# Performance work log

Hardware: AMD Instinct MI355X
Metric: run time of the kernel (lower is better)

## Reference

```python
import jax, jax.numpy as jnp
import numpy as np

STRIDE = 1
PAD = 1
DIL = 1


def setup_inputs() -> dict:
    key = jax.random.key(0)
    k1, k2, k3 = jax.random.split(key, 3)
    N, Cin, H, W = 8, 128, 96, 96
    Cout, Kh, Kw = 256, 3, 3
    inp = jax.random.normal(k1, (N, Cin, H, W), dtype=jnp.float32)
    # offset channels: 2*Kh*Kw per offset group (1 group), layout (dy, dx) pairs
    offset = jax.random.normal(k2, (N, 2 * Kh * Kw, H, W), dtype=jnp.float32)
    weight = jax.random.normal(k3, (Cout, Cin, Kh, Kw), dtype=jnp.float32) * 0.05
    return {"input": inp, "offset": offset, "weight": weight}


def _deform_conv(inp, offset, weight):
    N, Cin, H, W = inp.shape
    Cout, _, Kh, Kw = weight.shape
    K = Kh * Kw
    Ho = (H + 2 * PAD - DIL * (Kh - 1) - 1) // STRIDE + 1
    Wo = (W + 2 * PAD - DIL * (Kw - 1) - 1) // STRIDE + 1

    # base sampling grid (before learned offsets)
    hs = jnp.arange(Ho, dtype=inp.dtype) * STRIDE - PAD          # [Ho]
    ws = jnp.arange(Wo, dtype=inp.dtype) * STRIDE - PAD          # [Wo]
    ky, kx = jnp.meshgrid(jnp.arange(Kh, dtype=inp.dtype) * DIL,
                          jnp.arange(Kw, dtype=inp.dtype) * DIL,
                          indexing="ij")
    ky = ky.reshape(K)
    kx = kx.reshape(K)

    off = offset.reshape(N, K, 2, Ho, Wo)                        # pairs (dy, dx)
    py = hs[None, None, :, None] + ky[None, :, None, None] + off[:, :, 0]  # [N,K,Ho,Wo]
    px = ws[None, None, None, :] + kx[None, :, None, None] + off[:, :, 1]  # [N,K,Ho,Wo]

    y0 = jnp.floor(py)
    x0 = jnp.floor(px)
    ly = py - y0   # fractional parts
    lx = px - x0
    y0i = y0.astype(jnp.int32)
    x0i = x0.astype(jnp.int32)

    img = inp.transpose(0, 2, 3, 1)                              # [N,H,W,Cin]
    bidx = jnp.arange(N)[:, None, None, None]

    def gather(yi, xi):
        valid = (yi >= 0) & (yi < H) & (xi >= 0) & (xi < W)
        yc = jnp.clip(yi, 0, H - 1)
        xc = jnp.clip(xi, 0, W - 1)
        v = img[bidx, yc, xc]                                    # [N,K,Ho,Wo,Cin]
        return v * valid[..., None].astype(img.dtype)

    v00 = gather(y0i, x0i)
    v01 = gather(y0i, x0i + 1)
    v10 = gather(y0i + 1, x0i)
    v11 = gather(y0i + 1, x0i + 1)

    wy, wx = ly[..., None], lx[..., None]
    samp = (v00 * (1 - wy) * (1 - wx) + v01 * (1 - wy) * wx
            + v10 * wy * (1 - wx) + v11 * wy * wx)               # [N,K,Ho,Wo,Cin]

    w2 = weight.reshape(Cout, Cin, K)
    return jnp.einsum("nkhwc,ock->nohw", samp, w2)               # [N,Cout,Ho,Wo]


def reference(input, offset, weight):
    return _deform_conv(input, offset, weight)
```

## Files before the change

kernel.cpp:

```cpp
#include <hip/hip_runtime.h>
#include <hip/hip_bf16.h>

#define NN   8
#define CIN  128
#define HH   96
#define WW   96
#define COUT 256
#define KK   9
#define HO   96
#define WO   96
#define PTOT (NN*HO*WO)
#define BM   64
#define KTOT (CIN*KK)
#define KSTEPS (KTOT/32)

typedef short bf16x8 __attribute__((ext_vector_type(8)));
typedef float f32x4  __attribute__((ext_vector_type(4)));
typedef float f32x2  __attribute__((ext_vector_type(2)));

__device__ __forceinline__ float blo(unsigned u) { return __uint_as_float(u << 16); }
__device__ __forceinline__ float bhi(unsigned u) { return __uint_as_float(u & 0xffff0000u); }
__device__ __forceinline__ f32x2 unpk(unsigned u) {
    f32x2 r;
    r.x = __uint_as_float(u << 16);
    r.y = __uint_as_float(u & 0xffff0000u);
    return r;
}
__device__ __forceinline__ unsigned pack_bf2(float a, float b) {
    unsigned ua = __float_as_uint(a); ua += 0x7fffu + ((ua >> 16) & 1u);
    unsigned ub = __float_as_uint(b); ub += 0x7fffu + ((ub >> 16) & 1u);
    return (ua >> 16) | (ub & 0xffff0000u);
}
__device__ __forceinline__ unsigned short f2b(float a) {
    unsigned ua = __float_as_uint(a); ua += 0x7fffu + ((ua >> 16) & 1u);
    return (unsigned short)(ua >> 16);
}

__global__ __launch_bounds__(256) void to_nhwc_bf16(const float* __restrict__ in,
                                                    unsigned short* __restrict__ outp) {
    __shared__ float tile[CIN * 97];
    const int ny = blockIdx.x;
    const int n = ny / HH, y = ny - n * HH;
    const float* src = in + (size_t)n * CIN * HH * WW + (size_t)y * WW;
    for (int i = threadIdx.x; i < CIN * WW; i += 256) {
        int c = i / WW, x = i - c * WW;
        tile[c * 97 + x] = src[(size_t)c * HH * WW + x];
    }
    __syncthreads();
    unsigned* dst = (unsigned*)(outp + (size_t)ny * WW * CIN);
    for (int i = threadIdx.x; i < (WW * CIN) / 2; i += 256) {
        int c2 = (i & 63) * 2;
        int x  = i >> 6;
        dst[x * (CIN / 2) + (c2 >> 1)] = pack_bf2(tile[c2 * 97 + x], tile[(c2 + 1) * 97 + x]);
    }
}

__global__ __launch_bounds__(256) void w_pack(const float* __restrict__ w,
                                              unsigned short* __restrict__ wp) {
    int idx = blockIdx.x * 256 + threadIdx.x;
    if (idx >= KSTEPS * 16 * 64 * 8) return;
    int j  = idx & 7;
    int l  = (idx >> 3) & 63;
    int cb = (idx >> 9) & 15;
    int ks = idx >> 13;
    int co  = cb * 16 + (l & 15);
    int kg  = ks * 32 + ((l >> 4) * 8) + j;
    int tap = kg >> 7;
    int cin = kg & 127;
    wp[idx] = f2b(w[((size_t)co * CIN + cin) * KK + tap]);
}

#define GEOM_BYTES 6912
#define LDS_BYTES  39680
#define BUF0 6912
#define BUF1 23296

__global__ __launch_bounds__(256, 4) void deform_mfma(
    const unsigned short* __restrict__ imgB,
    const float*          __restrict__ off,
    const unsigned short* __restrict__ wPack,
    float*                __restrict__ out)
{
    __shared__ __align__(16) char smem[LDS_BYTES];
    unsigned* gOff = (unsigned*)smem;
    unsigned* gW0  = (unsigned*)(smem + 2304);
    unsigned* gW1  = (unsigned*)(smem + 4608);

    const int t    = threadIdx.x;
    const int lane = t & 63;
    const int wv   = t >> 6;

    const int bid  = ((blockIdx.x & 7) * ((PTOT / BM) >> 3)) + (blockIdx.x >> 3);

    const int p0   = bid * BM;
    const int nb   = p0 / (HO * WO);
    const int p0rem = p0 - nb * (HO * WO);

    for (int i = t; i < KK * BM; i += 256) {
        int tap = i >> 6, m = i & 63;
        int plin = p0rem + m;
        int ho = plin / WO, wo = plin - ho * WO;
        int kh = tap / 3, kw = tap - kh * 3;
        const float* ob = off + ((size_t)nb * 2 * KK + 2 * tap) * (HO * WO) + plin;
        float py = (float)(ho - 1 + kh) + ob[0];
        float px = (float)(wo - 1 + kw) + ob[HO * WO];
        float y0f = floorf(py), x0f = floorf(px);
        float ly = py - y0f, lx = px - x0f;
        int y0 = (int)y0f, x0 = (int)x0f;

        bool vy0 = (unsigned)y0 < (unsigned)HH;
        bool vy1 = (unsigned)(y0 + 1) < (unsigned)HH;
        bool vx0 = (unsigned)x0 < (unsigned)WW;
        bool vx1 = (unsigned)(x0 + 1) < (unsigned)WW;
        int yc0 = min(max(y0, 0), HH - 1);
        int yc1 = min(max(y0 + 1, 0), HH - 1);
        int xc0 = min(max(x0, 0), WW - 1);
        int xc1 = min(max(x0 + 1, 0), WW - 1);

        float w11 = ly * lx;
        float w10 = ly - w11;
        float w01 = lx - w11;
        float w00 = 1.f - ly - lx + w11;
        w00 = (vy0 && vx0) ? w00 : 0.f;
        w01 = (vy0 && vx1) ? w01 : 0.f;
        w10 = (vy1 && vx0) ? w10 : 0.f;
        w11 = (vy1 && vx1) ? w11 : 0.f;

        unsigned byte00 = (unsigned)(yc0 * WW + xc0) * (CIN * 2);
        unsigned xs = (xc1 != xc0) ? 1u : 0u;
        unsigned ys = (yc1 != yc0) ? 1u : 0u;
        gOff[i] = byte00 | (xs << 22) | (ys << 23);
        gW0[i]  = pack_bf2(w00, w01);
        gW1[i]  = pack_bf2(w10, w11);
    }

    f32x4 acc[4][4];
#pragma unroll
    for (int mf = 0; mf < 4; ++mf)
#pragma unroll
        for (int nf = 0; nf < 4; ++nf) acc[mf][nf] = (f32x4)0.f;

    const char* imgN = (const char*)(imgB + (size_t)nb * (HH * WW) * CIN);

    auto gather = [&](int tap, char* bufw) {
#pragma unroll
        for (int it = 0; it < 4; ++it) {
            int item  = t + it * 256;
            int pos   = item >> 4;
            int chunk = item & 15;
            int gi    = tap * 64 + pos;

            unsigned ofl  = gOff[gi];
            unsigned w0pk = gW0[gi];
            unsigned w1pk = gW1[gi];

            unsigned a00 = (ofl & 0x3fffffu) + (unsigned)(chunk * 16);
            unsigned dx  = (ofl >> 14) & 0x100u;
            unsigned dy  = ((ofl >> 23) & 1u) * 24576u;

            uint4 r00 = *(const uint4*)(imgN + a00);
            uint4 r01 = *(const uint4*)(imgN + a00 + dx);
            uint4 r10 = *(const uint4*)(imgN + a00 + dy);
            uint4 r11 = *(const uint4*)(imgN + a00 + dy + dx);

            float w00 = blo(w0pk), w01 = bhi(w0pk);
            float w10 = blo(w1pk), w11 = bhi(w1pk);

            unsigned pk[4];
            f32x2 s;
            s = unpk(r00.x) * w00 + unpk(r01.x) * w01 + unpk(r10.x) * w10 + unpk(r11.x) * w11;
            pk[0] = pack_bf2(s.x, s.y);
            s = unpk(r00.y) * w00 + unpk(r01.y) * w01 + unpk(r10.y) * w10 + unpk(r11.y) * w11;
            pk[1] = pack_bf2(s.x, s.y);
            s = unpk(r00.z) * w00 + unpk(r01.z) * w01 + unpk(r10.z) * w10 + unpk(r11.z) * w11;
            pk[2] = pack_bf2(s.x, s.y);
            s = unpk(r00.w) * w00 + unpk(r01.w) * w01 + unpk(r10.w) * w10 + unpk(r11.w) * w11;
            pk[3] = pack_bf2(s.x, s.y);

            int byte = pos * 256 + chunk * 16;
            byte ^= (pos & 7) << 4;
            *(uint4*)(bufw + byte) = make_uint4(pk[0], pk[1], pk[2], pk[3]);
        }
    };

    __syncthreads();
    gather(0, smem + BUF0);

    for (int tap = 0; tap < KK; ++tap) {
        __syncthreads();
        const char* bufr = smem + ((tap & 1) ? BUF1 : BUF0);

#pragma unroll
        for (int cs = 0; cs < 4; ++cs) {
            int ks = tap * 4 + cs;
            bf16x8 a[4], b[4];
#pragma unroll
            for (int mf = 0; mf < 4; ++mf) {
                int row  = mf * 16 + (lane & 15);
                int byte = row * 256 + cs * 64 + ((lane >> 4) * 16);
                byte ^= (row & 7) << 4;
                a[mf] = *(const bf16x8*)(bufr + byte);
            }
#pragma unroll
            for (int nf = 0; nf < 4; ++nf) {
                int tile = ks * 16 + (wv * 4 + nf);
                b[nf] = *(const bf16x8*)(wPack + (size_t)tile * 512 + lane * 8);
            }
            __builtin_amdgcn_s_setprio(1);
#pragma unroll
            for (int mf = 0; mf < 4; ++mf)
#pragma unroll
                for (int nf = 0; nf < 4; ++nf)
                    acc[mf][nf] = __builtin_amdgcn_mfma_f32_16x16x32_bf16(
                        a[mf], b[nf], acc[mf][nf], 0, 0, 0);
            __builtin_amdgcn_s_setprio(0);
        }

        if (tap + 1 < KK) gather(tap + 1, smem + ((tap & 1) ? BUF0 : BUF1));
    }

    __syncthreads();
    float* cT = (float*)smem + wv * (64 * 20);
    const int colbase = lane & 15;
    const int rowq    = lane >> 4;
    float* outbase = out + ((size_t)nb * COUT + wv * 64 + lane) * (HO * WO) + p0rem;
#pragma unroll
    for (int mf = 0; mf < 4; ++mf) {
#pragma unroll
        for (int nf = 0; nf < 4; ++nf) {
            int co = nf * 16 + colbase;
            *(f32x4*)&cT[co * 20 + rowq * 4] = acc[mf][nf];
        }
        asm volatile("s_waitcnt lgkmcnt(0)" ::: "memory");
        __builtin_amdgcn_sched_barrier(0);
#pragma unroll
        for (int q = 0; q < 4; ++q) {
            f32x4 v = *(f32x4*)&cT[lane * 20 + q * 4];
            *(float4*)(outbase + mf * 16 + q * 4) = *(float4*)&v;
        }
    }
}

__global__ __launch_bounds__(256) void deform_fallback(const float* __restrict__ img,
                                                       const float* __restrict__ off,
                                                       const float* __restrict__ wgt,
                                                       float* __restrict__ out) {
    __shared__ float samp[8][CIN];
    const int tid = threadIdx.x;
    const int p0  = blockIdx.x * 8;
    const int n   = p0 / (HO * WO);
    const int rem = p0 % (HO * WO);
    const int ho  = rem / WO;
    const int wo0 = rem % WO;
    float acc[8];
#pragma unroll
    for (int t = 0; t < 8; ++t) acc[t] = 0.f;
    for (int k = 0; k < KK; ++k) {
        __syncthreads();
        const int kh = k / 3, kw = k % 3;
#pragma unroll
        for (int it = 0; it < 4; ++it) {
            int idx = tid + it * 256;
            int t   = idx >> 7;
            int c   = idx & (CIN - 1);
            int wo  = wo0 + t;
            float dy = off[(((size_t)n * 2 * KK + 2 * k) * HO + ho) * WO + wo];
            float dx = off[(((size_t)n * 2 * KK + 2 * k + 1) * HO + ho) * WO + wo];
            float py = (float)(ho - 1 + kh) + dy;
            float px = (float)(wo - 1 + kw) + dx;
            float y0f = floorf(py), x0f = floorf(px);
            float ly = py - y0f, lx = px - x0f;
            int y0 = (int)y0f, x0 = (int)x0f;
            float v00 = 0.f, v01 = 0.f, v10 = 0.f, v11 = 0.f;
            const float* base = img + ((size_t)n * CIN + c) * HH * WW;
            if ((unsigned)y0 < (unsigned)HH) {
                const float* row = base + (size_t)y0 * WW;
                if ((unsigned)x0 < (unsigned)WW)       v00 = row[x0];
                if ((unsigned)(x0 + 1) < (unsigned)WW) v01 = row[x0 + 1];
            }
            if ((unsigned)(y0 + 1) < (unsigned)HH) {
                const float* row = base + (size_t)(y0 + 1) * WW;
                if ((unsigned)x0 < (unsigned)WW)       v10 = row[x0];
                if ((unsigned)(x0 + 1) < (unsigned)WW) v11 = row[x0 + 1];
            }
            float top = v00 + lx * (v01 - v00);
            float bot = v10 + lx * (v11 - v10);
            samp[t][c] = top + ly * (bot - top);
        }
        __syncthreads();
        const float* wk = wgt + (size_t)tid * CIN * KK + k;
        for (int c = 0; c < CIN; c += 4) {
            float w0 = wk[(c + 0) * KK], w1 = wk[(c + 1) * KK];
            float w2 = wk[(c + 2) * KK], w3 = wk[(c + 3) * KK];
#pragma unroll
            for (int t = 0; t < 8; ++t) {
                const float4 s = *(const float4*)&samp[t][c];
                acc[t] = fmaf(s.x, w0, acc[t]);
                acc[t] = fmaf(s.y, w1, acc[t]);
                acc[t] = fmaf(s.z, w2, acc[t]);
                acc[t] = fmaf(s.w, w3, acc[t]);
            }
        }
    }
#pragma unroll
    for (int t = 0; t < 8; ++t)
        out[(((size_t)n * COUT + tid) * HO + ho) * WO + wo0 + t] = acc[t];
}

extern "C" void kernel_launch(void* const* d_in, const int* in_sizes, int n_in,
                              void* d_out, int out_size, void* d_ws, size_t ws_size,
                              hipStream_t stream) {
    const float* inp = (const float*)d_in[0];
    const float* off = (const float*)d_in[1];
    const float* wgt = (const float*)d_in[2];
    float* out = (float*)d_out;

    const size_t img_bytes = (size_t)NN * HH * WW * CIN * 2;
    const size_t wp_bytes  = (size_t)KSTEPS * 16 * 64 * 8 * 2;

    if (ws_size >= img_bytes + wp_bytes) {
        unsigned short* imgB  = (unsigned short*)d_ws;
        unsigned short* wPack = (unsigned short*)((char*)d_ws + img_bytes);
        to_nhwc_bf16<<<NN * HH, 256, 0, stream>>>(inp, imgB);
        w_pack<<<(KSTEPS * 16 * 64 * 8) / 256, 256, 0, stream>>>(wgt, wPack);
        deform_mfma<<<PTOT / BM, 256, 0, stream>>>(imgB, off, wPack, out);
    } else {
        deform_fallback<<<PTOT / 8, 256, 0, stream>>>(inp, off, wgt, out);
    }
}
```

Baseline: 110.8 us.

## Interleave next-tap bilinear gather loads with current-tap MFMA chunks

Splits the bilinear gather into an issue phase (global corner loads) and a finish phase (interpolate and store to LDS). It then interleaves them with the four MFMA sub-steps of the current tap, so global load latency overlaps matrix math instead of running after it. The cost is more live registers, since a Corners struct of four uint4 values stays in flight across MFMA blocks, which may hurt occupancy under the launch bounds of 4 blocks.

```diff
diff --git a/kernel.cpp b/kernel.cpp
--- a/kernel.cpp
+++ b/kernel.cpp
@@ -75,6 +75,12 @@
 #define BUF0 6912
 #define BUF1 23296
 
+struct Corners {
+    uint4 r00, r01, r10, r11;
+    unsigned w0, w1;
+    int byte;
+};
+
 __global__ __launch_bounds__(256, 4) void deform_mfma(
     const unsigned short* __restrict__ imgB,
     const float*          __restrict__ off,
@@ -142,81 +148,93 @@
 
     const char* imgN = (const char*)(imgB + (size_t)nb * (HH * WW) * CIN);
 
-    auto gather = [&](int tap, char* bufw) {
-#pragma unroll
-        for (int it = 0; it < 4; ++it) {
-            int item  = t + it * 256;
-            int pos   = item >> 4;
-            int chunk = item & 15;
-            int gi    = tap * 64 + pos;
-
-            unsigned ofl  = gOff[gi];
-            unsigned w0pk = gW0[gi];
-            unsigned w1pk = gW1[gi];
-
-            unsigned a00 = (ofl & 0x3fffffu) + (unsigned)(chunk * 16);
-            unsigned dx  = (ofl >> 14) & 0x100u;
-            unsigned dy  = ((ofl >> 23) & 1u) * 24576u;
-
-            uint4 r00 = *(const uint4*)(imgN + a00);
-            uint4 r01 = *(const uint4*)(imgN + a00 + dx);
-            uint4 r10 = *(const uint4*)(imgN + a00 + dy);
-            uint4 r11 = *(const uint4*)(imgN + a00 + dy + dx);
-
-            float w00 = blo(w0pk), w01 = bhi(w0pk);
-            float w10 = blo(w1pk), w11 = bhi(w1pk);
-
-            unsigned pk[4];
-            f32x2 s;
-            s = unpk(r00.x) * w00 + unpk(r01.x) * w01 + unpk(r10.x) * w10 + unpk(r11.x) * w11;
-            pk[0] = pack_bf2(s.x, s.y);
-            s = unpk(r00.y) * w00 + unpk(r01.y) * w01 + unpk(r10.y) * w10 + unpk(r11.y) * w11;
-            pk[1] = pack_bf2(s.x, s.y);
-            s = unpk(r00.z) * w00 + unpk(r01.z) * w01 + unpk(r10.z) * w10 + unpk(r11.z) * w11;
-            pk[2] = pack_bf2(s.x, s.y);
-            s = unpk(r00.w) * w00 + unpk(r01.w) * w01 + unpk(r10.w) * w10 + unpk(r11.w) * w11;
-            pk[3] = pack_bf2(s.x, s.y);
-
-            int byte = pos * 256 + chunk * 16;
-            byte ^= (pos & 7) << 4;
-            *(uint4*)(bufw + byte) = make_uint4(pk[0], pk[1], pk[2], pk[3]);
-        }
+    auto issue = [&](int tap, int it) -> Corners {
+        Corners c;
+        int item  = t + it * 256;
+        int pos   = item >> 4;
+        int chunk = item & 15;
+        int gi    = tap * 64 + pos;
+        unsigned ofl = gOff[gi];
+        c.w0 = gW0[gi];
+        c.w1 = gW1[gi];
+        unsigned a00 = (ofl & 0x3fffffu) + (unsigned)(chunk * 16);
+        unsigned dx  = (ofl >> 14) & 0x100u;
+        unsigned dy  = ((ofl >> 23) & 1u) * 24576u;
+        c.r00 = *(const uint4*)(imgN + a00);
+        c.r01 = *(const uint4*)(imgN + a00 + dx);
+        c.r10 = *(const uint4*)(imgN + a00 + dy);
+        c.r11 = *(const uint4*)(imgN + a00 + dy + dx);
+        int byte = pos * 256 + chunk * 16;
+        byte ^= (pos & 7) << 4;
+        c.byte = byte;
+        return c;
     };
 
+    auto finish = [&](const Corners& c, char* bufw) {
+        float w00 = blo(c.w0), w01 = bhi(c.w0);
+        float w10 = blo(c.w1), w11 = bhi(c.w1);
+        unsigned pk[4];
+        f32x2 s;
+        s = unpk(c.r00.x) * w00 + unpk(c.r01.x) * w01 + unpk(c.r10.x) * w10 + unpk(c.r11.x) * w11;
+        pk[0] = pack_bf2(s.x, s.y);
+        s = unpk(c.r00.y) * w00 + unpk(c.r01.y) * w01 + unpk(c.r10.y) * w10 + unpk(c.r11.y) * w11;
+        pk[1] = pack_bf2(s.x, s.y);
+        s = unpk(c.r00.z) * w00 + unpk(c.r01.z) * w01 + unpk(c.r10.z) * w10 + unpk(c.r11.z) * w11;
+        pk[2] = pack_bf2(s.x, s.y);
+        s = unpk(c.r00.w) * w00 + unpk(c.r01.w) * w01 + unpk(c.r10.w) * w10 + unpk(c.r11.w) * w11;
+        pk[3] = pack_bf2(s.x, s.y);
+        *(uint4*)(bufw + c.byte) = make_uint4(pk[0], pk[1], pk[2], pk[3]);
+    };
+
+    auto mfma_cs = [&](int tap, int cs, const char* bufr) {
+        int ks = tap * 4 + cs;
+        bf16x8 a[4], b[4];
+#pragma unroll
+        for (int mf = 0; mf < 4; ++mf) {
+            int row  = mf * 16 + (lane & 15);
+            int byte = row * 256 + cs * 64 + ((lane >> 4) * 16);
+            byte ^= (row & 7) << 4;
+            a[mf] = *(const bf16x8*)(bufr + byte);
+        }
+#pragma unroll
+        for (int nf = 0; nf < 4; ++nf) {
+            int tile = ks * 16 + (wv * 4 + nf);
+            b[nf] = *(const bf16x8*)(wPack + (size_t)tile * 512 + lane * 8);
+        }
+        __builtin_amdgcn_s_setprio(1);
+#pragma unroll
+        for (int mf = 0; mf < 4; ++mf)
+#pragma unroll
+            for (int nf = 0; nf < 4; ++nf)
+                acc[mf][nf] = __builtin_amdgcn_mfma_f32_16x16x32_bf16(
+                    a[mf], b[nf], acc[mf][nf], 0, 0, 0);
+        __builtin_amdgcn_s_setprio(0);
+    };
+
     __syncthreads();
-    gather(0, smem + BUF0);
+
+#pragma unroll
+    for (int it = 0; it < 4; ++it) {
+        Corners c = issue(0, it);
+        finish(c, smem + BUF0);
+    }
 
     for (int tap = 0; tap < KK; ++tap) {
         __syncthreads();
         const char* bufr = smem + ((tap & 1) ? BUF1 : BUF0);
-
-#pragma unroll
-        for (int cs = 0; cs < 4; ++cs) {
-            int ks = tap * 4 + cs;
-            bf16x8 a[4], b[4];
-#pragma unroll
-            for (int mf = 0; mf < 4; ++mf) {
-                int row  = mf * 16 + (lane & 15);
-                int byte = row * 256 + cs * 64 + ((lane >> 4) * 16);
-                byte ^= (row & 7) << 4;
-                a[mf] = *(const bf16x8*)(bufr + byte);
-            }
-#pragma unroll
-            for (int nf = 0; nf < 4; ++nf) {
-                int tile = ks * 16 + (wv * 4 + nf);
-                b[nf] = *(const bf16x8*)(wPack + (size_t)tile * 512 + lane * 8);
-            }
-            __builtin_amdgcn_s_setprio(1);
-#pragma unroll
-            for (int mf = 0; mf < 4; ++mf)
-#pragma unroll
-                for (int nf = 0; nf < 4; ++nf)
-                    acc[mf][nf] = __builtin_amdgcn_mfma_f32_16x16x32_bf16(
-                        a[mf], b[nf], acc[mf][nf], 0, 0, 0);
-            __builtin_amdgcn_s_setprio(0);
-        }
-
-        if (tap + 1 < KK) gather(tap + 1, smem + ((tap & 1) ? BUF0 : BUF1));
+        char*       bufw = smem + ((tap & 1) ? BUF0 : BUF1);
+        const bool  pf   = (tap + 1 < KK);
+
+        Corners c;
+        if (pf) c = issue(tap + 1, 0);
+        mfma_cs(tap, 0, bufr);
+        if (pf) { finish(c, bufw); c = issue(tap + 1, 1); }
+        mfma_cs(tap, 1, bufr);
+        if (pf) { finish(c, bufw); c = issue(tap + 1, 2); }
+        mfma_cs(tap, 2, bufr);
+        if (pf) { finish(c, bufw); c = issue(tap + 1, 3); }
+        mfma_cs(tap, 3, bufr);
+        if (pf) finish(c, bufw);
     }
 
     __syncthreads();
```

After: 138.4 us. 1.25x slower.
